# Performance work log

Hardware: AMD Instinct MI355X
Metric: run time of the kernel (lower is better)

## Reference

```python
import jax, jax.numpy as jnp
import numpy as np

OBS_DIM = 64; ACT_DIM = 18; INTER = 64; COMMAND = 32
UNITS = ACT_DIM + COMMAND + INTER  # 114; neuron order: [motor, command, inter]
Q_HIDDEN = max(32, UNITS)
B, T = 2048, 64
ODE_UNFOLDS = 6
EPS = 1e-8


def _build_wiring(seed=0):
    """NCP sparse wiring: sensory->inter, inter->command, command recurrent, command->motor."""
    rng = np.random.default_rng(seed)
    adj = np.zeros((UNITS, UNITS), np.float32)   # [pre, post]
    sens = np.zeros((OBS_DIM, UNITS), np.float32)
    motor = np.arange(ACT_DIM)
    cmd = np.arange(ACT_DIM, ACT_DIM + COMMAND)
    inter = np.arange(ACT_DIM + COMMAND, UNITS)
    for s in range(OBS_DIM):
        for d in rng.choice(inter, size=8, replace=False):
            sens[s, d] = rng.choice([-1.0, 1.0])
    for i in inter:
        for d in rng.choice(cmd, size=8, replace=False):
            adj[i, d] = rng.choice([-1.0, 1.0])
    for _ in range(32):
        adj[rng.choice(cmd), rng.choice(cmd)] = rng.choice([-1.0, 1.0])
    for m in motor:
        for s in rng.choice(cmd, size=8, replace=False):
            adj[s, m] = rng.choice([-1.0, 1.0])
    return adj, sens


def setup_inputs() -> dict:
    key = jax.random.key(0)
    ks = jax.random.split(key, 16)
    adj, sens = _build_wiring()
    u = lambda k, shape, lo, hi: jax.random.uniform(k, shape, jnp.float32, lo, hi)
    return {
        "obs": jax.random.normal(ks[0], (B, T, OBS_DIM), jnp.float32),
        "hidden": jnp.zeros((B, UNITS), jnp.float32),
        "input_w": jnp.ones((OBS_DIM,), jnp.float32),
        "input_b": jnp.zeros((OBS_DIM,), jnp.float32),
        "sensory_w": u(ks[1], (OBS_DIM, UNITS), 0.001, 1.0),
        "sensory_mu": u(ks[2], (OBS_DIM, UNITS), 0.3, 0.8),
        "sensory_sigma": u(ks[3], (OBS_DIM, UNITS), 3.0, 8.0),
        "sensory_erev": jnp.asarray(sens),
        "sensory_mask": jnp.asarray(np.abs(sens)),
        "w": u(ks[4], (UNITS, UNITS), 0.001, 1.0),
        "mu": u(ks[5], (UNITS, UNITS), 0.3, 0.8),
        "sigma": u(ks[6], (UNITS, UNITS), 3.0, 8.0),
        "erev": jnp.asarray(adj),
        "mask": jnp.asarray(np.abs(adj)),
        "gleak": u(ks[7], (UNITS,), 0.001, 1.0),
        "vleak": u(ks[8], (UNITS,), -0.2, 0.2),
        "cm": u(ks[9], (UNITS,), 0.4, 0.6),
        "q_w1": jax.random.normal(ks[10], (UNITS, Q_HIDDEN), jnp.float32) / np.sqrt(UNITS).astype(np.float32),
        "q_b1": jnp.zeros((Q_HIDDEN,), jnp.float32),
        "q_w2": jax.random.normal(ks[11], (Q_HIDDEN, ACT_DIM), jnp.float32) / np.sqrt(Q_HIDDEN).astype(np.float32),
        "q_b2": jnp.zeros((ACT_DIM,), jnp.float32),
    }


def _ltc_forward(obs, hidden, input_w, input_b, sensory_w, sensory_mu, sensory_sigma,
                 sensory_erev, sensory_mask, w, mu, sigma, erev, mask, gleak, vleak, cm):
    sw = sensory_w * sensory_mask          # sparse sensory synapses (S, U)
    ww = w * mask                          # sparse recurrent synapses (U, U)
    cm_t = cm * ODE_UNFOLDS                # cm / (elapsed_time / ode_unfolds), elapsed_time = 1.0

    @jax.checkpoint
    def step(h, x):
        xi = x * input_w + input_b                                                    # (B, S) affine input map
        s_act = sw * jax.nn.sigmoid((xi[:, :, None] - sensory_mu) * sensory_sigma)    # (B, S, U)
        w_num_s = jnp.sum(s_act * sensory_erev, axis=1)                               # (B, U)
        w_den_s = jnp.sum(s_act, axis=1)                                              # (B, U)

        def unfold(v, _):
            act = ww * jax.nn.sigmoid((v[:, :, None] - mu) * sigma)                   # (B, U, U)
            num = cm_t * v + gleak * vleak + jnp.sum(act * erev, axis=1) + w_num_s
            den = cm_t + gleak + jnp.sum(act, axis=1) + w_den_s
            return num / (den + EPS), None

        v, _ = jax.lax.scan(unfold, h, None, length=ODE_UNFOLDS)
        return v, None

    h, _ = jax.lax.scan(step, hidden, jnp.swapaxes(obs, 0, 1))  # scan over time
    return h


def reference(obs, hidden, input_w, input_b, sensory_w, sensory_mu, sensory_sigma,
              sensory_erev, sensory_mask, w, mu, sigma, erev, mask, gleak, vleak, cm,
              q_w1, q_b1, q_w2, q_b2):
    h = _ltc_forward(obs, hidden, input_w, input_b, sensory_w, sensory_mu, sensory_sigma,
                     sensory_erev, sensory_mask, w, mu, sigma, erev, mask, gleak, vleak, cm)
    q = jax.nn.relu(h @ q_w1 + q_b1) @ q_w2 + q_b2  # Q-head over full hidden state
    return q, h
```

## Files before the change

### kernel.cpp

```cpp
#include <hip/hip_runtime.h>

#define UNITS   114
#define SDIM    64
#define ACT     18
#define TSTEPS  64

#define CR 13
#define CS 9
#define ER_CAP 704
#define MSTRIDE 24

#define LOG2E 1.4426950408889634f
#define EPS   1e-8f

typedef float v2f __attribute__((ext_vector_type(2)));
__device__ __forceinline__ v2f fma2(v2f a, v2f b, v2f c) {
  return __builtin_elementwise_fma(a, b, c);
}
__device__ __forceinline__ float bperm(int addr, float v) {
  return __int_as_float(__builtin_amdgcn_ds_bpermute(addr, __float_as_int(v)));
}
__device__ __forceinline__ float dperm(int addr, float v) {
  return __int_as_float(__builtin_amdgcn_ds_permute(addr, __float_as_int(v)));
}
__device__ __forceinline__ void wsync() {
  __builtin_amdgcn_fence(__ATOMIC_ACQ_REL, "wavefront");
  __builtin_amdgcn_wave_barrier();
}
__device__ __forceinline__ int canonLane(int u) { return (u >= 64) ? (u - 64) : u; }

__device__ __forceinline__ int kthSetBit(unsigned long long m, int k) {
  int pos = 0;
#pragma unroll
  for (int ww = 32; ww >= 1; ww >>= 1) {
    const unsigned long long lowMask = ((1ull << ww) - 1ull);
    const int c = __popcll(m & lowMask);
    if (k >= c) { k -= c; m >>= ww; pos += ww; }
  }
  return pos;
}

__global__ __launch_bounds__(64) void build_all(
    const float* __restrict__ w,  const float* __restrict__ mu,
    const float* __restrict__ sigma, const float* __restrict__ erev,
    const float* __restrict__ mask,
    const float* __restrict__ sw, const float* __restrict__ smu,
    const float* __restrict__ ssg, const float* __restrict__ serev,
    const float* __restrict__ smask,
    float4* __restrict__ recP4, float2* __restrict__ recP2, int* __restrict__ recAd,
    float4* __restrict__ senP4, float2* __restrict__ senP2, int* __restrict__ senAd,
    int* __restrict__ meta)
{
  const int l = threadIdx.x;
  __shared__ short ePre[ER_CAP], ePIdx[ER_CAP];
  __shared__ int deg[64], off[65];
  __shared__ int pLane[64], pF0[64], pRole[64];
  __shared__ int contIdx[64], contOwn[64], splitRole[64], split2[64], ownP[128];
  __shared__ int rcv[64];

  contIdx[l] = 0; contOwn[l] = 0; splitRole[l] = -1; split2[l] = 0;
  ownP[2*l] = -1; ownP[2*l+1] = -1;
  pLane[l] = 0; pF0[l] = 0; pRole[l] = 0;

  if (blockIdx.x == 0) {
    int d = 0;
    if (l < 50) {
      for (int base = 18; base < 114; base += 16) {
        float mv[16];
#pragma unroll
        for (int q = 0; q < 16; ++q) mv[q] = mask[(base + q)*UNITS + l];
#pragma unroll
        for (int q = 0; q < 16; ++q) d += (mv[q] != 0.f) ? 1 : 0;
      }
    }
    deg[l] = (l < 50) ? d : 0;
    __syncthreads();
    if (l == 0) { int a = 0; for (int j = 0; j < 64; ++j) { off[j] = a; a += deg[j]; } off[64] = a; }
    __syncthreads();
    if (l < 50) {
      int o = off[l];
      for (int base = 18; base < 114; base += 16) {
        float mv[16];
#pragma unroll
        for (int q = 0; q < 16; ++q) mv[q] = mask[(base + q)*UNITS + l];
#pragma unroll
        for (int q = 0; q < 16; ++q)
          if (mv[q] != 0.f) { ePre[o] = (short)(base + q); ePIdx[o] = (short)l; ++o; }
      }
    }
    if (l == 0) {
      int lam = 0, f = 0, pc = 0;
      for (int p = 0; p < 50; ++p) {
        const int dd = deg[p];
        if (pc == 2 || f == CR || dd > 3*CR - f) { ++lam; f = 0; pc = 0; }
        if (lam > 63) lam = 63;
        pLane[p] = lam; pF0[p] = f; pRole[p] = pc;
        ownP[2*lam + pc] = p;
        const int owner = lam, role = pc; ++pc;
        const int take = dd < (CR - f) ? dd : (CR - f);
        f += take; int rem = dd - take;
        if (rem > 0) {
          splitRole[owner] = role; split2[owner] = (rem > CR) ? 1 : 0;
          ++lam; if (lam > 63) lam = 63; contIdx[lam] = 1; contOwn[lam] = owner; pc = 1;
          const int t2 = rem < CR ? rem : CR; f = t2; rem -= t2;
          if (rem > 0) { ++lam; if (lam > 63) lam = 63; contIdx[lam] = 2; contOwn[lam] = owner; pc = 1; f = rem; }
        }
      }
    }
    __syncthreads();
    int dA = (contIdx[l] == 1) ? contOwn[l] : -1;
    int dB = (contIdx[l] == 2) ? contOwn[l] : -1;
    rcv[l] = 0; __syncthreads();
    if (dA >= 0) rcv[dA] = 1;
    __syncthreads();
    { const unsigned long long rM = __ballot(rcv[l] != 0), dM = __ballot(dA < 0);
      if (dA < 0) dA = kthSetBit(~rM, __popcll(dM & ((1ull << l) - 1ull))); }
    __syncthreads();
    rcv[l] = 0; __syncthreads();
    if (dB >= 0) rcv[dB] = 1;
    __syncthreads();
    { const unsigned long long rM = __ballot(rcv[l] != 0), dM = __ballot(dB < 0);
      if (dB < 0) dB = kthSetBit(~rM, __popcll(dM & ((1ull << l) - 1ull))); }
    {
      int* M = meta + l * MSTRIDE;
      M[0] = dA * 4; M[1] = dB * 4;
      const float s1A = (splitRole[l] == 0) ? 1.f : 0.f, s1B = (splitRole[l] == 1) ? 1.f : 0.f;
      M[2] = __float_as_int(s1A); M[3] = __float_as_int(s1B);
      const float s2 = split2[l] ? 1.f : 0.f;
      M[4] = __float_as_int(s1A * s2); M[5] = __float_as_int(s1B * s2);
      const int uA = ownP[2*l], uB = ownP[2*l+1];
      M[6] = ((uA >= 0) ? uA : 128 + l) * 4;
      M[7] = ((uB >= 0) ? uB : 192 + l) * 4;
      M[8] = (uA >= 0) ? uA : 0;
      M[9] = (uB >= 0) ? uB : 0;
    }
    for (int t = l; t < CR*64; t += 64) {
      recP4[t] = make_float4(0.f,0.f,0.f,0.f); recP2[t] = make_float2(0.f,0.f); recAd[t] = 0;
    }
    __syncthreads();
    {
      const int E = off[64];
      for (int e = l; e < E; e += 64) {
        const int pre = ePre[e], pj = ePIdx[e];
        const int r  = e - off[pj];
        const int dd = deg[pj], f0 = pF0[pj], role0 = pRole[pj];
        const int take = dd < (CR - f0) ? dd : (CR - f0);
        int lane = pLane[pj], slot, role;
        if (r < take)            { slot = f0 + r;        role = role0; }
        else if (r < take + CR)  { lane += 1; slot = r - take;      role = 0; }
        else                     { lane += 2; slot = r - take - CR; role = 0; }
        if (lane > 63) lane = 63;
        const int idx = pre * UNITS + pj;
        const float sg = sigma[idx];
        const float nsgl = -sg * LOG2E, msl = mu[idx] * sg * LOG2E;
        const float wd = w[idx], wn = wd * erev[idx];
        const int tt = slot * 64 + lane;
        recP4[tt] = make_float4(nsgl, msl, role ? 0.f : wn, role ? 0.f : wd);
        recP2[tt] = role ? make_float2(wn, wd) : make_float2(0.f, 0.f);
        recAd[tt] = pre * 4;
      }
    }
  } else {
    int d = 0;
    {
      const int col = 50 + l;
      for (int base = 0; base < 64; base += 16) {
        float mv[16];
#pragma unroll
        for (int q = 0; q < 16; ++q) mv[q] = smask[(base + q)*UNITS + col];
#pragma unroll
        for (int q = 0; q < 16; ++q) d += (mv[q] != 0.f) ? 1 : 0;
      }
    }
    deg[l] = d;
    __syncthreads();
    if (l == 0) { int a = 0; for (int j = 0; j < 64; ++j) { off[j] = a; a += deg[j]; } off[64] = a; }
    __syncthreads();
    {
      int o = off[l]; const int col = 50 + l;
      for (int base = 0; base < 64; base += 16) {
        float mv[16];
#pragma unroll
        for (int q = 0; q < 16; ++q) mv[q] = smask[(base + q)*UNITS + col];
#pragma unroll
        for (int q = 0; q < 16; ++q)
          if (mv[q] != 0.f) { ePre[o] = (short)(base + q); ePIdx[o] = (short)l; ++o; }
      }
    }
    if (l == 0) {
      int lam = 0, f = 0, pc = 0;
      for (int p = 0; p < 64; ++p) {
        const int dd = deg[p];
        if (pc == 2 || f == CS || dd > 3*CS - f) { ++lam; f = 0; pc = 0; }
        if (lam > 63) lam = 63;
        pLane[p] = lam; pF0[p] = f; pRole[p] = pc;
        ownP[2*lam + pc] = p;
        const int owner = lam, role = pc; ++pc;
        const int take = dd < (CS - f) ? dd : (CS - f);
        f += take; int rem = dd - take;
        if (rem > 0) {
          splitRole[owner] = role; split2[owner] = (rem > CS) ? 1 : 0;
          ++lam; if (lam > 63) lam = 63; contIdx[lam] = 1; contOwn[lam] = owner; pc = 1;
          const int t2 = rem < CS ? rem : CS; f = t2; rem -= t2;
          if (rem > 0) { ++lam; if (lam > 63) lam = 63; contIdx[lam] = 2; contOwn[lam] = owner; pc = 1; f = rem; }
        }
      }
    }
    __syncthreads();
    int dA = (contIdx[l] == 1) ? contOwn[l] : -1;
    int dB = (contIdx[l] == 2) ? contOwn[l] : -1;
    rcv[l] = 0; __syncthreads();
    if (dA >= 0) rcv[dA] = 1;
    __syncthreads();
    { const unsigned long long rM = __ballot(rcv[l] != 0), dM = __ballot(dA < 0);
      if (dA < 0) dA = kthSetBit(~rM, __popcll(dM & ((1ull << l) - 1ull))); }
    __syncthreads();
    rcv[l] = 0; __syncthreads();
    if (dB >= 0) rcv[dB] = 1;
    __syncthreads();
    { const unsigned long long rM = __ballot(rcv[l] != 0), dM = __ballot(dB < 0);
      if (dB < 0) dB = kthSetBit(~rM, __popcll(dM & ((1ull << l) - 1ull))); }
    __syncthreads();
    int rA = (ownP[2*l]   >= 0) ? canonLane(50 + ownP[2*l])   : -1;
    int rB = (ownP[2*l+1] >= 0) ? canonLane(50 + ownP[2*l+1]) : -1;
    rcv[l] = 0; __syncthreads();
    if (rA >= 0) rcv[rA] = 1;
    __syncthreads();
    const int isRcvA = rcv[l];
    { const unsigned long long rM = __ballot(isRcvA != 0), dM = __ballot(rA < 0);
      if (rA < 0) rA = kthSetBit(~rM, __popcll(dM & ((1ull << l) - 1ull))); }
    __syncthreads();
    rcv[l] = 0; __syncthreads();
    if (rB >= 0) rcv[rB] = 1;
    __syncthreads();
    { const unsigned long long rM = __ballot(rcv[l] != 0), dM = __ballot(rB < 0);
      if (rB < 0) rB = kthSetBit(~rM, __popcll(dM & ((1ull << l) - 1ull))); }
    {
      int* M = meta + l * MSTRIDE;
      M[10] = dA * 4; M[11] = dB * 4;
      const float s1A = (splitRole[l] == 0) ? 1.f : 0.f, s1B = (splitRole[l] == 1) ? 1.f : 0.f;
      M[12] = __float_as_int(s1A); M[13] = __float_as_int(s1B);
      const float s2 = split2[l] ? 1.f : 0.f;
      M[14] = __float_as_int(s1A * s2); M[15] = __float_as_int(s1B * s2);
      M[16] = rA * 4; M[17] = rB * 4;
      M[18] = __float_as_int(isRcvA ? 1.f : 0.f);
      M[19] = __float_as_int(isRcvA ? 0.f : 1.f);
      const int pA = ownP[2*l], pB = ownP[2*l+1];
      M[20] = (pA >= 0) ? 50 + pA : 0;
      M[21] = (pB >= 0) ? 50 + pB : 0;
    }
    for (int t = l; t < CS*64; t += 64) {
      senP4[t] = make_float4(0.f,0.f,0.f,0.f); senP2[t] = make_float2(0.f,0.f); senAd[t] = 0;
    }
    __syncthreads();
    {
      const int E = off[64];
      for (int e = l; e < E; e += 64) {
        const int pre = ePre[e], pj = ePIdx[e];
        const int r  = e - off[pj];
        const int dd = deg[pj], f0 = pF0[pj], role0 = pRole[pj];
        const int take = dd < (CS - f0) ? dd : (CS - f0);
        int lane = pLane[pj], slot, role;
        if (r < take)            { slot = f0 + r;        role = role0; }
        else if (r < take + CS)  { lane += 1; slot = r - take;      role = 0; }
        else                     { lane += 2; slot = r - take - CS; role = 0; }
        if (lane > 63) lane = 63;
        const int col = 50 + pj;
        const int idx = pre * UNITS + col;
        const float sg = ssg[idx];
        const float nsgl = -sg * LOG2E, msl = smu[idx] * sg * LOG2E;
        const float wd = sw[idx], wn = wd * serev[idx];
        const int tt = slot * 64 + lane;
        senP4[tt] = make_float4(nsgl, msl, role ? 0.f : wn, role ? 0.f : wd);
        senP2[tt] = role ? make_float2(wn, wd) : make_float2(0.f, 0.f);
        senAd[tt] = pre * 4;
      }
    }
  }
}

__global__ __launch_bounds__(64, 2) void ltc_run(
    const float* __restrict__ obs,     const float* __restrict__ hidden,
    const float* __restrict__ input_w, const float* __restrict__ input_b,
    const float* __restrict__ gleak,   const float* __restrict__ vleak,
    const float* __restrict__ cm,
    const float* __restrict__ q_w1, const float* __restrict__ q_b1,
    const float* __restrict__ q_w2, const float* __restrict__ q_b2,
    const float4* __restrict__ recP4, const float2* __restrict__ recP2,
    const int* __restrict__ recAd,
    const float4* __restrict__ senP4, const float2* __restrict__ senP2,
    const int* __restrict__ senAd,
    const int* __restrict__ meta, float* __restrict__ out, int B)
{
  const int l = threadIdx.x, b = blockIdx.x;
  __shared__ float mirror[256];
  char* mbase = (char*)mirror;

  float rNS[CR], rMS[CR]; v2f rWA[CR], rWB[CR]; int rad[CR];
#pragma unroll
  for (int s = 0; s < CR; ++s) {
    const float4 p4 = recP4[s*64 + l]; const float2 p2 = recP2[s*64 + l];
    rNS[s] = p4.x; rMS[s] = p4.y; rWA[s] = (v2f){p4.z, p4.w};
    rWB[s] = (v2f){p2.x, p2.y}; rad[s] = recAd[s*64 + l];
  }
  float sNS[CS], sMS[CS]; v2f sWA[CS], sWB[CS]; int sad[CS];
#pragma unroll
  for (int s = 0; s < CS; ++s) {
    const float4 p4 = senP4[s*64 + l]; const float2 p2 = senP2[s*64 + l];
    sNS[s] = p4.x; sMS[s] = p4.y; sWA[s] = (v2f){p4.z, p4.w};
    sWB[s] = (v2f){p2.x, p2.y}; sad[s] = senAd[s*64 + l];
  }

  const int* M = meta + l * MSTRIDE;
  const int   rPush1 = M[0], rPush2 = M[1];
  const v2f gR1A = {__int_as_float(M[2]), __int_as_float(M[2])};
  const v2f gR1B = {__int_as_float(M[3]), __int_as_float(M[3])};
  const v2f gR2A = {__int_as_float(M[4]), __int_as_float(M[4])};
  const v2f gR2B = {__int_as_float(M[5]), __int_as_float(M[5])};
  const int   rWrA = M[6], rWrB = M[7], rUA = M[8], rUB = M[9];
  const int   sPush1 = M[10], sPush2 = M[11];
  const v2f gS1A = {__int_as_float(M[12]), __int_as_float(M[12])};
  const v2f gS1B = {__int_as_float(M[13]), __int_as_float(M[13])};
  const v2f gS2A = {__int_as_float(M[14]), __int_as_float(M[14])};
  const v2f gS2B = {__int_as_float(M[15]), __int_as_float(M[15])};
  const int   sRtA = M[16], sRtB = M[17];
  const float sRndA = __int_as_float(M[18]), sRndB = __int_as_float(M[19]);
  const int   sUA = M[20], sUB = M[21];

  const float cmA  = cm[rUA]*6.f, glvA  = gleak[rUA]*vleak[rUA], cgA  = cm[rUA]*6.f + gleak[rUA] + EPS;
  const float cmB  = cm[rUB]*6.f, glvB  = gleak[rUB]*vleak[rUB], cgB  = cm[rUB]*6.f + gleak[rUB] + EPS;
  const float cmSA = cm[sUA]*6.f, glvSA = gleak[sUA]*vleak[sUA], cgSA = cm[sUA]*6.f + gleak[sUA] + EPS;
  const float cmSB = cm[sUB]*6.f, glvSB = gleak[sUB]*vleak[sUB], cgSB = cm[sUB]*6.f + gleak[sUB] + EPS;

  const bool ownA  = (rWrA < 512), ownB  = (rWrB < 512);
  const bool ownSA = (sUA != 0),   ownSB = (sUB != 0);
  const v2f initRA = ownA  ? (v2f){glvA,  cgA}  : (v2f){0.f, EPS};
  const v2f initRB = ownB  ? (v2f){glvB,  cgB}  : (v2f){0.f, EPS};
  const v2f initSA = ownSA ? (v2f){glvSA, cgSA} : (v2f){0.f, EPS};
  const v2f initSB = ownSB ? (v2f){glvSB, cgSB} : (v2f){0.f, EPS};

  const int  iUnit = (l < 50) ? 64 + l : l;
  const int  iWr   = iUnit * 4;
  float vIn = hidden[(size_t)b*UNITS + iUnit];
  float vPA = hidden[(size_t)b*UNITS + rUA];
  float vPB = hidden[(size_t)b*UNITS + rUB];

  mirror[l] = hidden[(size_t)b*UNITS + l];
  if (l < 50) mirror[64 + l] = hidden[(size_t)b*UNITS + 64 + l];

  const float iw = input_w[l], ibv = input_b[l];
  const float* ob = obs + (size_t)b*(TSTEPS*SDIM) + l;

  float aI, bI;
  {
    const float xi = fmaf(ob[0], iw, ibv);
    float uu[CS];
#pragma unroll
    for (int s = 0; s < CS; ++s) {
      float z = fmaf(bperm(sad[s], xi), sNS[s], sMS[s]);
      z = fminf(z, 30.f);
      uu[s] = 1.f + __builtin_amdgcn_exp2f(z);
    }
    float sg[CS];
#pragma unroll
    for (int q = 0; q < 4; ++q) {
      const float p = uu[2*q] * uu[2*q+1];
      const float r = __builtin_amdgcn_rcpf(p);
      sg[2*q]   = uu[2*q+1] * r;
      sg[2*q+1] = uu[2*q]   * r;
    }
    sg[8] = __builtin_amdgcn_rcpf(uu[8]);
    v2f cA = {0.f,0.f}, cB = {0.f,0.f};
#pragma unroll
    for (int s = 0; s < CS; ++s) {
      const v2f s2 = {sg[s], sg[s]};
      cA = fma2(sWA[s], s2, cA);
      cB = fma2(sWB[s], s2, cB);
    }
    const v2f m1 = {dperm(sPush1, cA.x), dperm(sPush1, cA.y)};
    const v2f m2 = {dperm(sPush2, cA.x), dperm(sPush2, cA.y)};
    v2f tA = fma2(gS1A, m1, cA); tA = fma2(gS2A, m2, tA);
    v2f tB = fma2(gS1B, m1, cB); tB = fma2(gS2B, m2, tB);
    const float rdA = __builtin_amdgcn_rcpf(cgSA + tA.y);
    const float aA = cmSA * rdA, bA = (glvSA + tA.x) * rdA;
    const float rdB = __builtin_amdgcn_rcpf(cgSB + tB.y);
    const float aB = cmSB * rdB, bB = (glvSB + tB.x) * rdB;
    const float ra1 = dperm(sRtA, aA), rb1 = dperm(sRtA, bA);
    const float ra2 = dperm(sRtB, aB), rb2 = dperm(sRtB, bB);
    aI = sRndA*ra1 + sRndB*ra2;
    bI = sRndA*rb1 + sRndB*rb2;
  }

  float xiN = fmaf(ob[SDIM], iw, ibv);
  float xrC = ob[2*SDIM];
  float su[CS];
  v2f acA = initSA, acB = initSB;
  v2f tSA = {0.f,0.f}, tSB = {0.f,0.f};
  float aIn = 0.f, bIn = 0.f;

  auto unfold = [&](auto chunk) {
    wsync();
    float uu[CR];
#pragma unroll
    for (int s = 0; s < CR; ++s) {
      const float pv = *(const float*)(mbase + rad[s]);
      const float z = fmaf(pv, rNS[s], rMS[s]);
      uu[s] = 1.f + __builtin_amdgcn_exp2f(z);
    }
    chunk();
    float sg[CR];
#pragma unroll
    for (int q = 0; q < 5; ++q) {
      const float p = uu[2*q] * uu[2*q+1];
      const float r = __builtin_amdgcn_rcpf(p);
      sg[2*q]   = uu[2*q+1] * r;
      sg[2*q+1] = uu[2*q]   * r;
    }
    {
      const float p01 = uu[10]*uu[11];
      const float r = __builtin_amdgcn_rcpf(p01*uu[12]);
      const float t12 = uu[12]*r;
      sg[10] = uu[11]*t12; sg[11] = uu[10]*t12; sg[12] = p01*r;
    }
    v2f a0 = initRA, a1 = {0.f,0.f}, b0 = initRB, b1 = {0.f,0.f};
#pragma unroll
    for (int s = 0; s < CR; ++s) {
      const v2f s2 = {sg[s], sg[s]};
      if (s & 1) { a1 = fma2(rWA[s], s2, a1); b1 = fma2(rWB[s], s2, b1); }
      else       { a0 = fma2(rWA[s], s2, a0); b0 = fma2(rWB[s], s2, b0); }
    }
    v2f aA = a0 + a1, aB = b0 + b1;
    const v2f m1 = {dperm(rPush1, aA.x), dperm(rPush1, aA.y)};
    const v2f m2 = {dperm(rPush2, aA.x), dperm(rPush2, aA.y)};
    v2f tA = fma2(gR1A, m1, aA); tA = fma2(gR2A, m2, tA);
    v2f tB = fma2(gR1B, m1, aB); tB = fma2(gR2B, m2, tB);
    const float dAq = tA.y, dBq = tB.y;
    const float rr = __builtin_amdgcn_rcpf(dAq * dBq);
    vPA = fmaf(cmA, vPA, tA.x) * (dBq * rr);
    vPB = fmaf(cmB, vPB, tB.x) * (dAq * rr);
    vIn = fmaf(aI, vIn, bI);
    wsync();
    *(float*)(mbase + rWrA) = vPA;
    *(float*)(mbase + rWrB) = vPB;
    *(float*)(mbase + iWr)  = vIn;
  };

  auto sExp = [&](int s) {
    float z = fmaf(bperm(sad[s], xiN), sNS[s], sMS[s]);
    z = fminf(z, 30.f);
    su[s] = 1.f + __builtin_amdgcn_exp2f(z);
  };
  auto sPair = [&](int s0) {
    const float p = su[s0] * su[s0+1];
    const float r = __builtin_amdgcn_rcpf(p);
    const float g0 = su[s0+1] * r, g1 = su[s0] * r;
    acA = fma2(sWA[s0],   (v2f){g0,g0}, acA);
    acA = fma2(sWA[s0+1], (v2f){g1,g1}, acA);
    acB = fma2(sWB[s0],   (v2f){g0,g0}, acB);
    acB = fma2(sWB[s0+1], (v2f){g1,g1}, acB);
  };

#pragma unroll 1
  for (int t = 0; t < TSTEPS; ++t) {
    unfold([&]{ sExp(0); sExp(1); });
    unfold([&]{ sExp(2); sExp(3); sPair(0); });
    unfold([&]{ sExp(4); sExp(5); sPair(2); });
    unfold([&]{ sExp(6); sExp(7); sExp(8); sPair(4); });
    unfold([&]{
      const float p67 = su[6] * su[7];
      const float r = __builtin_amdgcn_rcpf(p67 * su[8]);
      const float t67 = su[8] * r;
      const float g6 = su[7]*t67, g7 = su[6]*t67, g8 = p67*r;
      acA = fma2(sWA[6], (v2f){g6,g6}, acA); acB = fma2(sWB[6], (v2f){g6,g6}, acB);
      acA = fma2(sWA[7], (v2f){g7,g7}, acA); acB = fma2(sWB[7], (v2f){g7,g7}, acB);
      acA = fma2(sWA[8], (v2f){g8,g8}, acA); acB = fma2(sWB[8], (v2f){g8,g8}, acB);
      const v2f m1 = {dperm(sPush1, acA.x), dperm(sPush1, acA.y)};
      const v2f m2 = {dperm(sPush2, acA.x), dperm(sPush2, acA.y)};
      tSA = fma2(gS1A, m1, acA); tSA = fma2(gS2A, m2, tSA);
      tSB = fma2(gS1B, m1, acB); tSB = fma2(gS2B, m2, tSB);
    });
    unfold([&]{
      const float dA_ = tSA.y, dB_ = tSB.y;
      const float rr = __builtin_amdgcn_rcpf(dA_ * dB_);
      const float rdA = dB_ * rr, rdB = dA_ * rr;
      const float aA = cmSA * rdA, bA = tSA.x * rdA;
      const float aB = cmSB * rdB, bB = tSB.x * rdB;
      const float ra1 = dperm(sRtA, aA), rb1 = dperm(sRtA, bA);
      const float ra2 = dperm(sRtB, aB), rb2 = dperm(sRtB, bB);
      aIn = sRndA*ra1 + sRndB*ra2;
      bIn = sRndA*rb1 + sRndB*rb2;
    });
    aI = aIn; bI = bIn;
    xiN = fmaf(xrC, iw, ibv);
    const int tn = (t + 3 < TSTEPS) ? (t + 3) : (TSTEPS - 1);
    xrC = ob[tn * SDIM];
    acA = initSA; acB = initSB;
  }
  wsync();

  float* __restrict__ outH = out + (size_t)B * ACT;
  outH[(size_t)b*UNITS + l] = mirror[l];
  if (l < 50) outH[(size_t)b*UNITS + 64 + l] = mirror[64 + l];

  const int j2 = (l < 50) ? 64 + l : l;
  float h1 = q_b1[l], h2 = q_b1[j2];
  for (int i = 0; i < UNITS; ++i) {
    const float hv = mirror[i];
    h1 = fmaf(hv, q_w1[i*UNITS + l],  h1);
    h2 = fmaf(hv, q_w1[i*UNITS + j2], h2);
  }
  h1 = fmaxf(h1, 0.f); h2 = fmaxf(h2, 0.f);
  wsync();
  mirror[l] = h1;
  if (l < 50) mirror[64 + l] = h2;
  wsync();
  if (l < ACT) {
    float q = q_b2[l];
    for (int i = 0; i < UNITS; ++i) q = fmaf(mirror[i], q_w2[i*ACT + l], q);
    out[(size_t)b*ACT + l] = q;
  }
}

extern "C" void kernel_launch(void* const* d_in, const int* in_sizes, int n_in,
                              void* d_out, int out_size, void* d_ws, size_t ws_size,
                              hipStream_t stream)
{
  const float* obs           = (const float*)d_in[0];
  const float* hidden        = (const float*)d_in[1];
  const float* input_w       = (const float*)d_in[2];
  const float* input_b       = (const float*)d_in[3];
  const float* sensory_w     = (const float*)d_in[4];
  const float* sensory_mu    = (const float*)d_in[5];
  const float* sensory_sigma = (const float*)d_in[6];
  const float* sensory_erev  = (const float*)d_in[7];
  const float* sensory_mask  = (const float*)d_in[8];
  const float* w             = (const float*)d_in[9];
  const float* mu            = (const float*)d_in[10];
  const float* sigma         = (const float*)d_in[11];
  const float* erev          = (const float*)d_in[12];
  const float* mask          = (const float*)d_in[13];
  const float* gleak         = (const float*)d_in[14];
  const float* vleak         = (const float*)d_in[15];
  const float* cm            = (const float*)d_in[16];
  const float* q_w1          = (const float*)d_in[17];
  const float* q_b1          = (const float*)d_in[18];
  const float* q_w2          = (const float*)d_in[19];
  const float* q_b2          = (const float*)d_in[20];

  char* ws = (char*)d_ws;
  float4* recP4 = (float4*)(ws);
  float2* recP2 = (float2*)(ws + 13312);
  int*    recAd = (int*)   (ws + 19968);
  float4* senP4 = (float4*)(ws + 23296);
  float2* senP2 = (float2*)(ws + 32512);
  int*    senAd = (int*)   (ws + 37120);
  int*    meta  = (int*)   (ws + 39424);

  build_all<<<2, 64, 0, stream>>>(
      w, mu, sigma, erev, mask,
      sensory_w, sensory_mu, sensory_sigma, sensory_erev, sensory_mask,
      recP4, recP2, recAd, senP4, senP2, senAd, meta);

  const int B = in_sizes[0] / (TSTEPS * SDIM);
  ltc_run<<<B, 64, 0, stream>>>(
      obs, hidden, input_w, input_b, gleak, vleak, cm,
      q_w1, q_b1, q_w2, q_b2,
      recP4, recP2, recAd, senP4, senP2, senAd, meta,
      (float*)d_out, B);
}
```

Measured before the change: 368.8 us.

## Fuse sparse-wiring build kernel into main LTC kernel, rebuilt per block

```diff
diff --git a/kernel.cpp b/kernel.cpp
--- a/kernel.cpp
+++ b/kernel.cpp
@@ -8,7 +8,6 @@
 #define CR 13
 #define CS 9
 #define ER_CAP 704
-#define MSTRIDE 24
 
 #define LOG2E 1.4426950408889634f
 #define EPS   1e-8f
@@ -40,292 +39,288 @@
   return pos;
 }
 
-__global__ __launch_bounds__(64) void build_all(
-    const float* __restrict__ w,  const float* __restrict__ mu,
-    const float* __restrict__ sigma, const float* __restrict__ erev,
-    const float* __restrict__ mask,
+__global__ __launch_bounds__(64, 2) void ltc_fused(
+    const float* __restrict__ obs,     const float* __restrict__ hidden,
+    const float* __restrict__ input_w, const float* __restrict__ input_b,
     const float* __restrict__ sw, const float* __restrict__ smu,
     const float* __restrict__ ssg, const float* __restrict__ serev,
     const float* __restrict__ smask,
-    float4* __restrict__ recP4, float2* __restrict__ recP2, int* __restrict__ recAd,
-    float4* __restrict__ senP4, float2* __restrict__ senP2, int* __restrict__ senAd,
-    int* __restrict__ meta)
+    const float* __restrict__ w, const float* __restrict__ mu,
+    const float* __restrict__ sigma, const float* __restrict__ erev,
+    const float* __restrict__ mask,
+    const float* __restrict__ gleak, const float* __restrict__ vleak,
+    const float* __restrict__ cm,
+    const float* __restrict__ q_w1, const float* __restrict__ q_b1,
+    const float* __restrict__ q_w2, const float* __restrict__ q_b2,
+    float* __restrict__ out, int B)
 {
-  const int l = threadIdx.x;
-  __shared__ short ePre[ER_CAP], ePIdx[ER_CAP];
-  __shared__ int deg[64], off[65];
+  const int l = threadIdx.x, b = blockIdx.x;
+  __shared__ float mirror[256];
+  __shared__ short ePre[ER_CAP];
+  __shared__ int offL[64], degL[64];
   __shared__ int pLane[64], pF0[64], pRole[64];
   __shared__ int contIdx[64], contOwn[64], splitRole[64], split2[64], ownP[128];
   __shared__ int rcv[64];
-
+  char* mbase = (char*)mirror;
+
+  mirror[l] = hidden[(size_t)b*UNITS + l];
+  if (l < 50) mirror[64 + l] = hidden[(size_t)b*UNITS + 64 + l];
+  const float iw = input_w[l], ibv = input_b[l];
+  const float* ob = obs + (size_t)b*(TSTEPS*SDIM) + l;
+
+  int d = 0;
+  if (l < 50) {
+    for (int base = 18; base < 114; base += 16) {
+      float mv[16];
+#pragma unroll
+      for (int q = 0; q < 16; ++q) mv[q] = mask[(base + q)*UNITS + l];
+#pragma unroll
+      for (int q = 0; q < 16; ++q) d += (mv[q] != 0.f) ? 1 : 0;
+    }
+  }
+  const int dregR = (l < 50) ? d : 0;
+  degL[l] = dregR;
+  int incl = dregR;
+#pragma unroll
+  for (int o = 1; o < 64; o <<= 1) { const int nn = __shfl_up(incl, o); if (l >= o) incl += nn; }
+  offL[l] = incl - dregR;
   contIdx[l] = 0; contOwn[l] = 0; splitRole[l] = -1; split2[l] = 0;
   ownP[2*l] = -1; ownP[2*l+1] = -1;
-  pLane[l] = 0; pF0[l] = 0; pRole[l] = 0;
-
-  if (blockIdx.x == 0) {
-    int d = 0;
-    if (l < 50) {
-      for (int base = 18; base < 114; base += 16) {
-        float mv[16];
-#pragma unroll
-        for (int q = 0; q < 16; ++q) mv[q] = mask[(base + q)*UNITS + l];
-#pragma unroll
-        for (int q = 0; q < 16; ++q) d += (mv[q] != 0.f) ? 1 : 0;
-      }
-    }
-    deg[l] = (l < 50) ? d : 0;
-    __syncthreads();
-    if (l == 0) { int a = 0; for (int j = 0; j < 64; ++j) { off[j] = a; a += deg[j]; } off[64] = a; }
-    __syncthreads();
-    if (l < 50) {
-      int o = off[l];
-      for (int base = 18; base < 114; base += 16) {
-        float mv[16];
-#pragma unroll
-        for (int q = 0; q < 16; ++q) mv[q] = mask[(base + q)*UNITS + l];
-#pragma unroll
-        for (int q = 0; q < 16; ++q)
-          if (mv[q] != 0.f) { ePre[o] = (short)(base + q); ePIdx[o] = (short)l; ++o; }
-      }
-    }
-    if (l == 0) {
-      int lam = 0, f = 0, pc = 0;
-      for (int p = 0; p < 50; ++p) {
-        const int dd = deg[p];
-        if (pc == 2 || f == CR || dd > 3*CR - f) { ++lam; f = 0; pc = 0; }
-        if (lam > 63) lam = 63;
-        pLane[p] = lam; pF0[p] = f; pRole[p] = pc;
-        ownP[2*lam + pc] = p;
-        const int owner = lam, role = pc; ++pc;
-        const int take = dd < (CR - f) ? dd : (CR - f);
-        f += take; int rem = dd - take;
+  wsync();
+  if (l < 50) {
+    int o = incl - dregR;
+    for (int base = 18; base < 114; base += 16) {
+      float mv[16];
+#pragma unroll
+      for (int q = 0; q < 16; ++q) mv[q] = mask[(base + q)*UNITS + l];
+#pragma unroll
+      for (int q = 0; q < 16; ++q)
+        if (mv[q] != 0.f) ePre[o++] = (short)(base + q);
+    }
+  }
+  wsync();
+  {
+    int lam = 0, f = 0, pc = 0;
+    for (int p = 0; p < 50; ++p) {
+      const int dd = __shfl(dregR, p);
+      if (pc == 2 || f == CR || dd > 3*CR - f) { ++lam; f = 0; pc = 0; }
+      if (lam > 63) lam = 63;
+      if (l == 0) { pLane[p] = lam; pF0[p] = f; pRole[p] = pc; ownP[2*lam + pc] = p; }
+      const int owner = lam, role = pc; ++pc;
+      const int take = dd < (CR - f) ? dd : (CR - f);
+      f += take; int rem = dd - take;
+      if (rem > 0) {
+        if (l == 0) { splitRole[owner] = role; split2[owner] = (rem > CR) ? 1 : 0; }
+        ++lam; if (lam > 63) lam = 63;
+        if (l == 0) { contIdx[lam] = 1; contOwn[lam] = owner; }
+        pc = 1;
+        const int t2 = rem < CR ? rem : CR; f = t2; rem -= t2;
         if (rem > 0) {
-          splitRole[owner] = role; split2[owner] = (rem > CR) ? 1 : 0;
-          ++lam; if (lam > 63) lam = 63; contIdx[lam] = 1; contOwn[lam] = owner; pc = 1;
-          const int t2 = rem < CR ? rem : CR; f = t2; rem -= t2;
-          if (rem > 0) { ++lam; if (lam > 63) lam = 63; contIdx[lam] = 2; contOwn[lam] = owner; pc = 1; f = rem; }
+          ++lam; if (lam > 63) lam = 63;
+          if (l == 0) { contIdx[lam] = 2; contOwn[lam] = owner; }
+          pc = 1; f = rem;
         }
       }
     }
-    __syncthreads();
-    int dA = (contIdx[l] == 1) ? contOwn[l] : -1;
-    int dB = (contIdx[l] == 2) ? contOwn[l] : -1;
-    rcv[l] = 0; __syncthreads();
-    if (dA >= 0) rcv[dA] = 1;
-    __syncthreads();
-    { const unsigned long long rM = __ballot(rcv[l] != 0), dM = __ballot(dA < 0);
-      if (dA < 0) dA = kthSetBit(~rM, __popcll(dM & ((1ull << l) - 1ull))); }
-    __syncthreads();
-    rcv[l] = 0; __syncthreads();
-    if (dB >= 0) rcv[dB] = 1;
-    __syncthreads();
-    { const unsigned long long rM = __ballot(rcv[l] != 0), dM = __ballot(dB < 0);
-      if (dB < 0) dB = kthSetBit(~rM, __popcll(dM & ((1ull << l) - 1ull))); }
-    {
-      int* M = meta + l * MSTRIDE;
-      M[0] = dA * 4; M[1] = dB * 4;
-      const float s1A = (splitRole[l] == 0) ? 1.f : 0.f, s1B = (splitRole[l] == 1) ? 1.f : 0.f;
-      M[2] = __float_as_int(s1A); M[3] = __float_as_int(s1B);
-      const float s2 = split2[l] ? 1.f : 0.f;
-      M[4] = __float_as_int(s1A * s2); M[5] = __float_as_int(s1B * s2);
-      const int uA = ownP[2*l], uB = ownP[2*l+1];
-      M[6] = ((uA >= 0) ? uA : 128 + l) * 4;
-      M[7] = ((uB >= 0) ? uB : 192 + l) * 4;
-      M[8] = (uA >= 0) ? uA : 0;
-      M[9] = (uB >= 0) ? uB : 0;
-    }
-    for (int t = l; t < CR*64; t += 64) {
-      recP4[t] = make_float4(0.f,0.f,0.f,0.f); recP2[t] = make_float2(0.f,0.f); recAd[t] = 0;
-    }
-    __syncthreads();
-    {
-      const int E = off[64];
-      for (int e = l; e < E; e += 64) {
-        const int pre = ePre[e], pj = ePIdx[e];
-        const int r  = e - off[pj];
-        const int dd = deg[pj], f0 = pF0[pj], role0 = pRole[pj];
-        const int take = dd < (CR - f0) ? dd : (CR - f0);
-        int lane = pLane[pj], slot, role;
-        if (r < take)            { slot = f0 + r;        role = role0; }
-        else if (r < take + CR)  { lane += 1; slot = r - take;      role = 0; }
-        else                     { lane += 2; slot = r - take - CR; role = 0; }
-        if (lane > 63) lane = 63;
-        const int idx = pre * UNITS + pj;
-        const float sg = sigma[idx];
-        const float nsgl = -sg * LOG2E, msl = mu[idx] * sg * LOG2E;
+  }
+  wsync();
+  int dAr = (contIdx[l] == 1) ? contOwn[l] : -1;
+  int dBr = (contIdx[l] == 2) ? contOwn[l] : -1;
+  rcv[l] = 0; wsync();
+  if (dAr >= 0) rcv[dAr] = 1;
+  wsync();
+  { const unsigned long long rM = __ballot(rcv[l] != 0), dM = __ballot(dAr < 0);
+    if (dAr < 0) dAr = kthSetBit(~rM, __popcll(dM & ((1ull << l) - 1ull))); }
+  wsync();
+  rcv[l] = 0; wsync();
+  if (dBr >= 0) rcv[dBr] = 1;
+  wsync();
+  { const unsigned long long rM = __ballot(rcv[l] != 0), dM = __ballot(dBr < 0);
+    if (dBr < 0) dBr = kthSetBit(~rM, __popcll(dM & ((1ull << l) - 1ull))); }
+  const int rPush1 = dAr * 4, rPush2 = dBr * 4;
+  const float s1Ar = (splitRole[l] == 0) ? 1.f : 0.f, s1Br = (splitRole[l] == 1) ? 1.f : 0.f;
+  const float s2r  = split2[l] ? 1.f : 0.f;
+  const v2f gR1A = {s1Ar, s1Ar}, gR1B = {s1Br, s1Br};
+  const v2f gR2A = {s1Ar*s2r, s1Ar*s2r}, gR2B = {s1Br*s2r, s1Br*s2r};
+  const int uA = ownP[2*l], uB = ownP[2*l+1];
+  const int rWrA = ((uA >= 0) ? uA : 128 + l) * 4;
+  const int rWrB = ((uB >= 0) ? uB : 192 + l) * 4;
+  const int rUA = (uA >= 0) ? uA : 0, rUB = (uB >= 0) ? uB : 0;
+  float rNS[CR], rMS[CR]; v2f rWA[CR], rWB[CR]; int rad[CR];
+  {
+    const int ci = contIdx[l];
+    int p1 = -1, base1 = 0, cnt1 = 0;
+    if (ci) {
+      const int o = contOwn[l];
+      p1 = ownP[2*o + splitRole[o]];
+      const int br = (CR - pF0[p1]) + ((ci == 2) ? CR : 0);
+      base1 = offL[p1] + br;
+      cnt1 = degL[p1] - br; if (cnt1 > CR) cnt1 = CR;
+    }
+    int fA = 0, tA = -1, oAo = 0;
+    if (uA >= 0) { fA = pF0[uA]; const int rm = CR - fA; const int dd = degL[uA];
+                   tA = dd < rm ? dd : rm; oAo = offL[uA]; }
+    int fB = 0, tB = -1, oBo = 0;
+    if (uB >= 0) { fB = pF0[uB]; const int rm = CR - fB; const int dd = degL[uB];
+                   tB = dd < rm ? dd : rm; oBo = offL[uB]; }
+#pragma unroll
+    for (int s = 0; s < CR; ++s) {
+      int e = -1, post = 0, isB = 0;
+      if (ci && s < cnt1)                          { e = base1 + s;      post = p1; }
+      else if (uA >= 0 && s >= fA && s < fA + tA)  { e = oAo + (s - fA); post = uA; }
+      else if (uB >= 0 && s >= fB && s < fB + tB)  { e = oBo + (s - fB); post = uB; isB = 1; }
+      if (e >= 0) {
+        const int pre = (int)ePre[e];
+        const int idx = pre * UNITS + post;
+        const float sg_ = sigma[idx];
+        rNS[s] = -sg_ * LOG2E; rMS[s] = mu[idx] * sg_ * LOG2E;
         const float wd = w[idx], wn = wd * erev[idx];
-        const int tt = slot * 64 + lane;
-        recP4[tt] = make_float4(nsgl, msl, role ? 0.f : wn, role ? 0.f : wd);
-        recP2[tt] = role ? make_float2(wn, wd) : make_float2(0.f, 0.f);
-        recAd[tt] = pre * 4;
+        rWA[s] = isB ? (v2f){0.f, 0.f} : (v2f){wn, wd};
+        rWB[s] = isB ? (v2f){wn, wd} : (v2f){0.f, 0.f};
+        rad[s] = pre * 4;
+      } else {
+        rNS[s] = 0.f; rMS[s] = 0.f;
+        rWA[s] = (v2f){0.f, 0.f}; rWB[s] = (v2f){0.f, 0.f};
+        rad[s] = 0;
       }
     }
-  } else {
-    int d = 0;
-    {
-      const int col = 50 + l;
-      for (int base = 0; base < 64; base += 16) {
-        float mv[16];
-#pragma unroll
-        for (int q = 0; q < 16; ++q) mv[q] = smask[(base + q)*UNITS + col];
-#pragma unroll
-        for (int q = 0; q < 16; ++q) d += (mv[q] != 0.f) ? 1 : 0;
-      }
-    }
-    deg[l] = d;
-    __syncthreads();
-    if (l == 0) { int a = 0; for (int j = 0; j < 64; ++j) { off[j] = a; a += deg[j]; } off[64] = a; }
-    __syncthreads();
-    {
-      int o = off[l]; const int col = 50 + l;
-      for (int base = 0; base < 64; base += 16) {
-        float mv[16];
-#pragma unroll
-        for (int q = 0; q < 16; ++q) mv[q] = smask[(base + q)*UNITS + col];
-#pragma unroll
-        for (int q = 0; q < 16; ++q)
-          if (mv[q] != 0.f) { ePre[o] = (short)(base + q); ePIdx[o] = (short)l; ++o; }
-      }
-    }
-    if (l == 0) {
-      int lam = 0, f = 0, pc = 0;
-      for (int p = 0; p < 64; ++p) {
-        const int dd = deg[p];
-        if (pc == 2 || f == CS || dd > 3*CS - f) { ++lam; f = 0; pc = 0; }
-        if (lam > 63) lam = 63;
-        pLane[p] = lam; pF0[p] = f; pRole[p] = pc;
-        ownP[2*lam + pc] = p;
-        const int owner = lam, role = pc; ++pc;
-        const int take = dd < (CS - f) ? dd : (CS - f);
-        f += take; int rem = dd - take;
+  }
+  wsync();
+
+  int ds_ = 0;
+  {
+    const int col = 50 + l;
+    for (int base = 0; base < 64; base += 16) {
+      float mv[16];
+#pragma unroll
+      for (int q = 0; q < 16; ++q) mv[q] = smask[(base + q)*UNITS + col];
+#pragma unroll
+      for (int q = 0; q < 16; ++q) ds_ += (mv[q] != 0.f) ? 1 : 0;
+    }
+  }
+  const int dregS = ds_;
+  degL[l] = dregS;
+  int inclS = dregS;
+#pragma unroll
+  for (int o = 1; o < 64; o <<= 1) { const int nn = __shfl_up(inclS, o); if (l >= o) inclS += nn; }
+  offL[l] = inclS - dregS;
+  contIdx[l] = 0; contOwn[l] = 0; splitRole[l] = -1; split2[l] = 0;
+  ownP[2*l] = -1; ownP[2*l+1] = -1;
+  wsync();
+  {
+    int o = inclS - dregS; const int col = 50 + l;
+    for (int base = 0; base < 64; base += 16) {
+      float mv[16];
+#pragma unroll
+      for (int q = 0; q < 16; ++q) mv[q] = smask[(base + q)*UNITS + col];
+#pragma unroll
+      for (int q = 0; q < 16; ++q)
+        if (mv[q] != 0.f) ePre[o++] = (short)(base + q);
+    }
+  }
+  wsync();
+  {
+    int lam = 0, f = 0, pc = 0;
+    for (int p = 0; p < 64; ++p) {
+      const int dd = __shfl(dregS, p);
+      if (pc == 2 || f == CS || dd > 3*CS - f) { ++lam; f = 0; pc = 0; }
+      if (lam > 63) lam = 63;
+      if (l == 0) { pLane[p] = lam; pF0[p] = f; pRole[p] = pc; ownP[2*lam + pc] = p; }
+      const int owner = lam, role = pc; ++pc;
+      const int take = dd < (CS - f) ? dd : (CS - f);
+      f += take; int rem = dd - take;
+      if (rem > 0) {
+        if (l == 0) { splitRole[owner] = role; split2[owner] = (rem > CS) ? 1 : 0; }
+        ++lam; if (lam > 63) lam = 63;
+        if (l == 0) { contIdx[lam] = 1; contOwn[lam] = owner; }
+        pc = 1;
+        const int t2 = rem < CS ? rem : CS; f = t2; rem -= t2;
         if (rem > 0) {
-          splitRole[owner] = role; split2[owner] = (rem > CS) ? 1 : 0;
-          ++lam; if (lam > 63) lam = 63; contIdx[lam] = 1; contOwn[lam] = owner; pc = 1;
-          const int t2 = rem < CS ? rem : CS; f = t2; rem -= t2;
-          if (rem > 0) { ++lam; if (lam > 63) lam = 63; contIdx[lam] = 2; contOwn[lam] = owner; pc = 1; f = rem; }
+          ++lam; if (lam > 63) lam = 63;
+          if (l == 0) { contIdx[lam] = 2; contOwn[lam] = owner; }
+          pc = 1; f = rem;
         }
       }
     }
-    __syncthreads();
-    int dA = (contIdx[l] == 1) ? contOwn[l] : -1;
-    int dB = (contIdx[l] == 2) ? contOwn[l] : -1;
-    rcv[l] = 0; __syncthreads();
-    if (dA >= 0) rcv[dA] = 1;
-    __syncthreads();
-    { const unsigned long long rM = __ballot(rcv[l] != 0), dM = __ballot(dA < 0);
-      if (dA < 0) dA = kthSetBit(~rM, __popcll(dM & ((1ull << l) - 1ull))); }
-    __syncthreads();
-    rcv[l] = 0; __syncthreads();
-    if (dB >= 0) rcv[dB] = 1;
-    __syncthreads();
-    { const unsigned long long rM = __ballot(rcv[l] != 0), dM = __ballot(dB < 0);
-      if (dB < 0) dB = kthSetBit(~rM, __popcll(dM & ((1ull << l) - 1ull))); }
-    __syncthreads();
-    int rA = (ownP[2*l]   >= 0) ? canonLane(50 + ownP[2*l])   : -1;
-    int rB = (ownP[2*l+1] >= 0) ? canonLane(50 + ownP[2*l+1]) : -1;
-    rcv[l] = 0; __syncthreads();
-    if (rA >= 0) rcv[rA] = 1;
-    __syncthreads();
-    const int isRcvA = rcv[l];
-    { const unsigned long long rM = __ballot(isRcvA != 0), dM = __ballot(rA < 0);
-      if (rA < 0) rA = kthSetBit(~rM, __popcll(dM & ((1ull << l) - 1ull))); }
-    __syncthreads();
-    rcv[l] = 0; __syncthreads();
-    if (rB >= 0) rcv[rB] = 1;
-    __syncthreads();
-    { const unsigned long long rM = __ballot(rcv[l] != 0), dM = __ballot(rB < 0);
-      if (rB < 0) rB = kthSetBit(~rM, __popcll(dM & ((1ull << l) - 1ull))); }
-    {
-      int* M = meta + l * MSTRIDE;
-      M[10] = dA * 4; M[11] = dB * 4;
-      const float s1A = (splitRole[l] == 0) ? 1.f : 0.f, s1B = (splitRole[l] == 1) ? 1.f : 0.f;
-      M[12] = __float_as_int(s1A); M[13] = __float_as_int(s1B);
-      const float s2 = split2[l] ? 1.f : 0.f;
-      M[14] = __float_as_int(s1A * s2); M[15] = __float_as_int(s1B * s2);
-      M[16] = rA * 4; M[17] = rB * 4;
-      M[18] = __float_as_int(isRcvA ? 1.f : 0.f);
-      M[19] = __float_as_int(isRcvA ? 0.f : 1.f);
-      const int pA = ownP[2*l], pB = ownP[2*l+1];
-      M[20] = (pA >= 0) ? 50 + pA : 0;
-      M[21] = (pB >= 0) ? 50 + pB : 0;
-    }
-    for (int t = l; t < CS*64; t += 64) {
-      senP4[t] = make_float4(0.f,0.f,0.f,0.f); senP2[t] = make_float2(0.f,0.f); senAd[t] = 0;
-    }
-    __syncthreads();
-    {
-      const int E = off[64];
-      for (int e = l; e < E; e += 64) {
-        const int pre = ePre[e], pj = ePIdx[e];
-        const int r  = e - off[pj];
-        const int dd = deg[pj], f0 = pF0[pj], role0 = pRole[pj];
-        const int take = dd < (CS - f0) ? dd : (CS - f0);
-        int lane = pLane[pj], slot, role;
-        if (r < take)            { slot = f0 + r;        role = role0; }
-        else if (r < take + CS)  { lane += 1; slot = r - take;      role = 0; }
-        else                     { lane += 2; slot = r - take - CS; role = 0; }
-        if (lane > 63) lane = 63;
-        const int col = 50 + pj;
-        const int idx = pre * UNITS + col;
-        const float sg = ssg[idx];
-        const float nsgl = -sg * LOG2E, msl = smu[idx] * sg * LOG2E;
+  }
+  wsync();
+  int dAs = (contIdx[l] == 1) ? contOwn[l] : -1;
+  int dBs = (contIdx[l] == 2) ? contOwn[l] : -1;
+  rcv[l] = 0; wsync();
+  if (dAs >= 0) rcv[dAs] = 1;
+  wsync();
+  { const unsigned long long rM = __ballot(rcv[l] != 0), dM = __ballot(dAs < 0);
+    if (dAs < 0) dAs = kthSetBit(~rM, __popcll(dM & ((1ull << l) - 1ull))); }
+  wsync();
+  rcv[l] = 0; wsync();
+  if (dBs >= 0) rcv[dBs] = 1;
+  wsync();
+  { const unsigned long long rM = __ballot(rcv[l] != 0), dM = __ballot(dBs < 0);
+    if (dBs < 0) dBs = kthSetBit(~rM, __popcll(dM & ((1ull << l) - 1ull))); }
+  wsync();
+  int rAs = (ownP[2*l]   >= 0) ? canonLane(50 + ownP[2*l])   : -1;
+  int rBs = (ownP[2*l+1] >= 0) ? canonLane(50 + ownP[2*l+1]) : -1;
+  rcv[l] = 0; wsync();
+  if (rAs >= 0) rcv[rAs] = 1;
+  wsync();
+  const int isRcvA = rcv[l];
+  { const unsigned long long rM = __ballot(isRcvA != 0), dM = __ballot(rAs < 0);
+    if (rAs < 0) rAs = kthSetBit(~rM, __popcll(dM & ((1ull << l) - 1ull))); }
+  wsync();
+  rcv[l] = 0; wsync();
+  if (rBs >= 0) rcv[rBs] = 1;
+  wsync();
+  { const unsigned long long rM = __ballot(rcv[l] != 0), dM = __ballot(rBs < 0);
+    if (rBs < 0) rBs = kthSetBit(~rM, __popcll(dM & ((1ull << l) - 1ull))); }
+  const int sPush1 = dAs * 4, sPush2 = dBs * 4;
+  const float s1As = (splitRole[l] == 0) ? 1.f : 0.f, s1Bs = (splitRole[l] == 1) ? 1.f : 0.f;
+  const float s2s  = split2[l] ? 1.f : 0.f;
+  const v2f gS1A = {s1As, s1As}, gS1B = {s1Bs, s1Bs};
+  const v2f gS2A = {s1As*s2s, s1As*s2s}, gS2B = {s1Bs*s2s, s1Bs*s2s};
+  const int sRtA = rAs * 4, sRtB = rBs * 4;
+  const float sRndA = isRcvA ? 1.f : 0.f, sRndB = isRcvA ? 0.f : 1.f;
+  const int pAs = ownP[2*l], pBs = ownP[2*l+1];
+  const int sUA = (pAs >= 0) ? 50 + pAs : 0;
+  const int sUB = (pBs >= 0) ? 50 + pBs : 0;
+  float sNS[CS], sMS[CS]; v2f sWA[CS], sWB[CS]; int sad[CS];
+  {
+    const int ci = contIdx[l];
+    int p1 = -1, base1 = 0, cnt1 = 0;
+    if (ci) {
+      const int o = contOwn[l];
+      p1 = ownP[2*o + splitRole[o]];
+      const int br = (CS - pF0[p1]) + ((ci == 2) ? CS : 0);
+      base1 = offL[p1] + br;
+      cnt1 = degL[p1] - br; if (cnt1 > CS) cnt1 = CS;
+    }
+    int fA = 0, tA = -1, oAo = 0;
+    if (pAs >= 0) { fA = pF0[pAs]; const int rm = CS - fA; const int dd = degL[pAs];
+                    tA = dd < rm ? dd : rm; oAo = offL[pAs]; }
+    int fB = 0, tB = -1, oBo = 0;
+    if (pBs >= 0) { fB = pF0[pBs]; const int rm = CS - fB; const int dd = degL[pBs];
+                    tB = dd < rm ? dd : rm; oBo = offL[pBs]; }
+#pragma unroll
+    for (int s = 0; s < CS; ++s) {
+      int e = -1, post = 0, isB = 0;
+      if (ci && s < cnt1)                           { e = base1 + s;      post = p1;  }
+      else if (pAs >= 0 && s >= fA && s < fA + tA)  { e = oAo + (s - fA); post = pAs; }
+      else if (pBs >= 0 && s >= fB && s < fB + tB)  { e = oBo + (s - fB); post = pBs; isB = 1; }
+      if (e >= 0) {
+        const int pre = (int)ePre[e];
+        const int idx = pre * UNITS + 50 + post;
+        const float sg_ = ssg[idx];
+        sNS[s] = -sg_ * LOG2E; sMS[s] = smu[idx] * sg_ * LOG2E;
         const float wd = sw[idx], wn = wd * serev[idx];
-        const int tt = slot * 64 + lane;
-        senP4[tt] = make_float4(nsgl, msl, role ? 0.f : wn, role ? 0.f : wd);
-        senP2[tt] = role ? make_float2(wn, wd) : make_float2(0.f, 0.f);
-        senAd[tt] = pre * 4;
+        sWA[s] = isB ? (v2f){0.f, 0.f} : (v2f){wn, wd};
+        sWB[s] = isB ? (v2f){wn, wd} : (v2f){0.f, 0.f};
+        sad[s] = pre * 4;
+      } else {
+        sNS[s] = 0.f; sMS[s] = 0.f;
+        sWA[s] = (v2f){0.f, 0.f}; sWB[s] = (v2f){0.f, 0.f};
+        sad[s] = 0;
       }
     }
   }
-}
-
-__global__ __launch_bounds__(64, 2) void ltc_run(
-    const float* __restrict__ obs,     const float* __restrict__ hidden,
-    const float* __restrict__ input_w, const float* __restrict__ input_b,
-    const float* __restrict__ gleak,   const float* __restrict__ vleak,
-    const float* __restrict__ cm,
-    const float* __restrict__ q_w1, const float* __restrict__ q_b1,
-    const float* __restrict__ q_w2, const float* __restrict__ q_b2,
-    const float4* __restrict__ recP4, const float2* __restrict__ recP2,
-    const int* __restrict__ recAd,
-    const float4* __restrict__ senP4, const float2* __restrict__ senP2,
-    const int* __restrict__ senAd,
-    const int* __restrict__ meta, float* __restrict__ out, int B)
-{
-  const int l = threadIdx.x, b = blockIdx.x;
-  __shared__ float mirror[256];
-  char* mbase = (char*)mirror;
-
-  float rNS[CR], rMS[CR]; v2f rWA[CR], rWB[CR]; int rad[CR];
-#pragma unroll
-  for (int s = 0; s < CR; ++s) {
-    const float4 p4 = recP4[s*64 + l]; const float2 p2 = recP2[s*64 + l];
-    rNS[s] = p4.x; rMS[s] = p4.y; rWA[s] = (v2f){p4.z, p4.w};
-    rWB[s] = (v2f){p2.x, p2.y}; rad[s] = recAd[s*64 + l];
-  }
-  float sNS[CS], sMS[CS]; v2f sWA[CS], sWB[CS]; int sad[CS];
-#pragma unroll
-  for (int s = 0; s < CS; ++s) {
-    const float4 p4 = senP4[s*64 + l]; const float2 p2 = senP2[s*64 + l];
-    sNS[s] = p4.x; sMS[s] = p4.y; sWA[s] = (v2f){p4.z, p4.w};
-    sWB[s] = (v2f){p2.x, p2.y}; sad[s] = senAd[s*64 + l];
-  }
-
-  const int* M = meta + l * MSTRIDE;
-  const int   rPush1 = M[0], rPush2 = M[1];
-  const v2f gR1A = {__int_as_float(M[2]), __int_as_float(M[2])};
-  const v2f gR1B = {__int_as_float(M[3]), __int_as_float(M[3])};
-  const v2f gR2A = {__int_as_float(M[4]), __int_as_float(M[4])};
-  const v2f gR2B = {__int_as_float(M[5]), __int_as_float(M[5])};
-  const int   rWrA = M[6], rWrB = M[7], rUA = M[8], rUB = M[9];
-  const int   sPush1 = M[10], sPush2 = M[11];
-  const v2f gS1A = {__int_as_float(M[12]), __int_as_float(M[12])};
-  const v2f gS1B = {__int_as_float(M[13]), __int_as_float(M[13])};
-  const v2f gS2A = {__int_as_float(M[14]), __int_as_float(M[14])};
-  const v2f gS2B = {__int_as_float(M[15]), __int_as_float(M[15])};
-  const int   sRtA = M[16], sRtB = M[17];
-  const float sRndA = __int_as_float(M[18]), sRndB = __int_as_float(M[19]);
-  const int   sUA = M[20], sUB = M[21];
 
   const float cmA  = cm[rUA]*6.f, glvA  = gleak[rUA]*vleak[rUA], cgA  = cm[rUA]*6.f + gleak[rUA] + EPS;
   const float cmB  = cm[rUB]*6.f, glvB  = gleak[rUB]*vleak[rUB], cgB  = cm[rUB]*6.f + gleak[rUB] + EPS;
@@ -344,12 +339,6 @@
   float vIn = hidden[(size_t)b*UNITS + iUnit];
   float vPA = hidden[(size_t)b*UNITS + rUA];
   float vPB = hidden[(size_t)b*UNITS + rUB];
-
-  mirror[l] = hidden[(size_t)b*UNITS + l];
-  if (l < 50) mirror[64 + l] = hidden[(size_t)b*UNITS + 64 + l];
-
-  const float iw = input_w[l], ibv = input_b[l];
-  const float* ob = obs + (size_t)b*(TSTEPS*SDIM) + l;
 
   float aI, bI;
   {
@@ -547,24 +536,12 @@
   const float* q_w2          = (const float*)d_in[19];
   const float* q_b2          = (const float*)d_in[20];
 
-  char* ws = (char*)d_ws;
-  float4* recP4 = (float4*)(ws);
-  float2* recP2 = (float2*)(ws + 13312);
-  int*    recAd = (int*)   (ws + 19968);
-  float4* senP4 = (float4*)(ws + 23296);
-  float2* senP2 = (float2*)(ws + 32512);
-  int*    senAd = (int*)   (ws + 37120);
-  int*    meta  = (int*)   (ws + 39424);
-
-  build_all<<<2, 64, 0, stream>>>(
+  const int B = in_sizes[0] / (TSTEPS * SDIM);
+  ltc_fused<<<B, 64, 0, stream>>>(
+      obs, hidden, input_w, input_b,
+      sensory_w, sensory_mu, sensory_sigma, sensory_erev, sensory_mask,
       w, mu, sigma, erev, mask,
-      sensory_w, sensory_mu, sensory_sigma, sensory_erev, sensory_mask,
-      recP4, recP2, recAd, senP4, senP2, senAd, meta);
-
-  const int B = in_sizes[0] / (TSTEPS * SDIM);
-  ltc_run<<<B, 64, 0, stream>>>(
-      obs, hidden, input_w, input_b, gleak, vleak, cm,
+      gleak, vleak, cm,
       q_w1, q_b1, q_w2, q_b2,
-      recP4, recP2, recAd, senP4, senP2, senAd, meta,
       (float*)d_out, B);
 }
```

Measured after the change: 388.4 us. 1.05x slower.
